# Optimization experiments

Hardware: AMD Instinct MI355X
Metric: run time of the kernel (lower is better)

Reference implementation:

```python
import jax, jax.numpy as jnp
import numpy as np


def setup_inputs() -> dict:
    key = jax.random.key(0)
    k1, k2, k3, k4 = jax.random.split(key, 4)
    N, E, IN, OUT = 100000, 1600000, 256, 32
    feat = jax.random.normal(k1, (N, IN), dtype=jnp.float32)
    src = jax.random.randint(k2, (E,), 0, N, dtype=jnp.int64)
    dst = jax.random.randint(k3, (E,), 0, N, dtype=jnp.int64)
    weight = jax.random.normal(k4, (IN, OUT), dtype=jnp.float32) * (6.0 / (IN + OUT)) ** 0.5
    bias = jnp.zeros((OUT,), dtype=jnp.float32)
    return {"feat": feat, "src": src, "dst": dst, "weight": weight, "bias": bias}


def reference(feat, src, dst, weight, bias):
    N = feat.shape[0]
    ones = jnp.ones(src.shape[0], dtype=feat.dtype)
    # norm='both': scale sources by out_degree^-0.5
    out_deg = jnp.clip(jax.ops.segment_sum(ones, src, num_segments=N), 1.0)
    feat = feat * (out_deg ** -0.5)[:, None]
    # in_feats (256) > out_feats (32): apply weight before aggregation
    feat = feat @ weight
    # SpMM: copy_src + sum over destination nodes
    rst = jax.ops.segment_sum(feat[src], dst, num_segments=N)  # [N, out]
    # scale destinations by in_degree^-0.5
    in_deg = jnp.clip(jax.ops.segment_sum(ones, dst, num_segments=N), 1.0)
    rst = rst * (in_deg ** -0.5)[:, None]
    rst = rst + bias
    return jax.nn.relu(rst)
```

## Files before the change

kernel.cpp:

```cpp
#include <hip/hip_runtime.h>
#include <hip/hip_bf16.h>


#define IN_F 256
#define OUT_F 32

#define G_ROWS 128
#define G_BK 32

#define BSHIFT 7
#define BNODES 128
#define NBK 1024
#define PB_EDGES 8192
#define AGG_CAP 4096


__global__ __launch_bounds__(1024) void hist_kernel(
    const int* __restrict__ src, const int* __restrict__ dst,
    unsigned short* __restrict__ mhistS, unsigned short* __restrict__ mhistD,
    int E) {
  __shared__ int hS[NBK], hD[NBK];
  int tid = threadIdx.x;
  hS[tid] = 0; hD[tid] = 0;
  __syncthreads();
  int e0 = blockIdx.x * PB_EDGES + tid * 8;
  if (e0 + 8 <= E) {
    int4 a0 = ((const int4*)(src + e0))[0], a1 = ((const int4*)(src + e0))[1];
    int4 b0 = ((const int4*)(dst + e0))[0], b1 = ((const int4*)(dst + e0))[1];
    int ss[8] = {a0.x, a0.y, a0.z, a0.w, a1.x, a1.y, a1.z, a1.w};
    int dd[8] = {b0.x, b0.y, b0.z, b0.w, b1.x, b1.y, b1.z, b1.w};
#pragma unroll
    for (int j = 0; j < 8; ++j) {
      atomicAdd(&hS[ss[j] >> BSHIFT], 1);
      atomicAdd(&hD[dd[j] >> BSHIFT], 1);
    }
  } else {
    for (int j = 0; j < 8; ++j) {
      int e = e0 + j;
      if (e < E) {
        atomicAdd(&hS[src[e] >> BSHIFT], 1);
        atomicAdd(&hD[dst[e] >> BSHIFT], 1);
      }
    }
  }
  __syncthreads();
  mhistS[blockIdx.x * NBK + tid] = (unsigned short)hS[tid];
  mhistD[blockIdx.x * NBK + tid] = (unsigned short)hD[tid];
}

__global__ __launch_bounds__(1024) void offset_kernel(
    unsigned short* __restrict__ mhistS, unsigned short* __restrict__ mhistD,
    int* __restrict__ baseS, int* __restrict__ baseD, int npb) {
  __shared__ int wsum[16];
  unsigned short* mh = blockIdx.x ? mhistD : mhistS;
  int* bb = blockIdx.x ? baseD : baseS;
  int b = threadIdx.x;
  int run = 0;
  int blk = 0;
  for (; blk + 4 <= npb; blk += 4) {
    int i0 = blk * NBK + b;
    int c0 = mh[i0];
    int c1 = mh[i0 + NBK];
    int c2 = mh[i0 + 2 * NBK];
    int c3 = mh[i0 + 3 * NBK];
    mh[i0] = (unsigned short)run;
    mh[i0 + NBK] = (unsigned short)(run + c0);
    mh[i0 + 2 * NBK] = (unsigned short)(run + c0 + c1);
    mh[i0 + 3 * NBK] = (unsigned short)(run + c0 + c1 + c2);
    run += c0 + c1 + c2 + c3;
  }
  for (; blk < npb; ++blk) {
    int idx = blk * NBK + b;
    int c = mh[idx];
    mh[idx] = (unsigned short)run;
    run += c;
  }
  int v = run, x = run;
#pragma unroll
  for (int d = 1; d < 64; d <<= 1) {
    int y = __shfl_up(x, d, 64);
    if ((b & 63) >= d) x += y;
  }
  if ((b & 63) == 63) wsum[b >> 6] = x;
  __syncthreads();
  int off = 0;
#pragma unroll
  for (int w = 0; w < 16; ++w)
    if (w < (b >> 6)) off += wsum[w];
  bb[b] = off + x - v;
  if (b == NBK - 1) bb[NBK] = off + x;
}

__global__ __launch_bounds__(1024) void partition_src_kernel(
    const int* __restrict__ src, const unsigned short* __restrict__ mbaseS,
    const int* __restrict__ baseS, unsigned char* __restrict__ pairs_s, int E) {
  __shared__ unsigned char sbuf[PB_EDGES];
  __shared__ int hist[NBK];
  __shared__ int lbase[NBK + 1];
  __shared__ int gbase[NBK];
  __shared__ int wsum[16];

  int tid = threadIdx.x;
  hist[tid] = 0;
  __syncthreads();

  int e0 = blockIdx.x * PB_EDGES + tid * 8;
  int myb[8], myslot[8];
  unsigned char mylow[8];
  if (e0 + 8 <= E) {
    int4 a0 = ((const int4*)(src + e0))[0], a1 = ((const int4*)(src + e0))[1];
    int ss[8] = {a0.x, a0.y, a0.z, a0.w, a1.x, a1.y, a1.z, a1.w};
#pragma unroll
    for (int j = 0; j < 8; ++j) {
      int b = ss[j] >> BSHIFT;
      myb[j] = b;
      mylow[j] = (unsigned char)(ss[j] & (BNODES - 1));
      myslot[j] = atomicAdd(&hist[b], 1);
    }
  } else {
#pragma unroll
    for (int j = 0; j < 8; ++j) {
      int e = e0 + j;
      if (e < E) {
        int s = src[e];
        int b = s >> BSHIFT;
        myb[j] = b;
        mylow[j] = (unsigned char)(s & (BNODES - 1));
        myslot[j] = atomicAdd(&hist[b], 1);
      } else {
        myb[j] = -1;
      }
    }
  }
  __syncthreads();

  {
    int v = hist[tid];
    int x = v;
#pragma unroll
    for (int d = 1; d < 64; d <<= 1) {
      int y = __shfl_up(x, d, 64);
      if ((tid & 63) >= d) x += y;
    }
    if ((tid & 63) == 63) wsum[tid >> 6] = x;
    __syncthreads();
    int off = 0;
#pragma unroll
    for (int w = 0; w < 16; ++w)
      if (w < (tid >> 6)) off += wsum[w];
    lbase[tid] = off + x - v;
    if (tid == NBK - 1) lbase[NBK] = off + x;
    gbase[tid] = baseS[tid] + (int)mbaseS[blockIdx.x * NBK + tid];
  }
  __syncthreads();

#pragma unroll
  for (int j = 0; j < 8; ++j)
    if (myb[j] >= 0) sbuf[lbase[myb[j]] + myslot[j]] = mylow[j];
  __syncthreads();

  int total = lbase[NBK];
  int idx = tid * 8;
  if (idx < total) {
    int lo = 0, hi = NBK;
    while (hi - lo > 1) {
      int mid = (lo + hi) >> 1;
      if (lbase[mid] <= idx) lo = mid; else hi = mid;
    }
    int b = lo;
#pragma unroll
    for (int j = 0; j < 8; ++j, ++idx) {
      if (idx >= total) break;
      while (idx >= lbase[b + 1]) ++b;
      pairs_s[gbase[b] + (idx - lbase[b])] = sbuf[idx];
    }
  }
}

__global__ __launch_bounds__(256) void src_count_kernel(
    const unsigned char* __restrict__ pairs_s, const int* __restrict__ baseS,
    float* __restrict__ scale_out, int N) {
  __shared__ int hist[BNODES];
  int tid = threadIdx.x;
  int b = blockIdx.x;
  if (tid < BNODES) hist[tid] = 0;
  __syncthreads();
  int s = baseS[b], e = baseS[b + 1];
  for (int i = s + tid; i < e; i += 256) atomicAdd(&hist[pairs_s[i]], 1);
  __syncthreads();
  if (tid < BNODES) {
    int node = (b << BSHIFT) + tid;
    if (node < N) {
      int c = hist[tid];
      scale_out[node] = (c < 1) ? 1.f : rsqrtf((float)c);
    }
  }
}

__device__ __forceinline__ void stage_tile(
    const float* __restrict__ feat, float* sf, int row0, int k0, int N,
    int tid) {
#pragma unroll
  for (int q = 0; q < 4; ++q) {
    int p = q * 256 + tid;
    int row = p >> 3;
    int c = (p & 7) ^ (row & 7);
    int g = row0 + row;
    if (g >= N) g = N - 1;
    const float* gp = feat + (size_t)g * IN_F + k0 + c * 4;
    __builtin_amdgcn_global_load_lds(
        (const __attribute__((address_space(1))) unsigned int*)gp,
        (__attribute__((address_space(3))) unsigned int*)(sf + p * 4),
        16, 0, 0);
  }
}

__global__ __launch_bounds__(256, 2) void gemm_kernel(
    const float* __restrict__ feat, const float* __restrict__ W,
    const float* __restrict__ scale_out, float* __restrict__ h, int N) {
  __shared__ float sW[IN_F * OUT_F];
  __shared__ float sF[2][G_ROWS * G_BK];
  __shared__ float sScale[G_ROWS];

  int tid = threadIdx.x;
  {
    const float4* W4 = (const float4*)W;
    float4* sW4 = (float4*)sW;
#pragma unroll
    for (int i = 0; i < 8; ++i) sW4[tid + i * 256] = W4[tid + i * 256];
  }
  int row0 = blockIdx.x * G_ROWS;
  if (tid < G_ROWS) {
    int gr = row0 + tid;
    sScale[tid] = (gr < N) ? scale_out[gr] : 0.f;
  }

  stage_tile(feat, &sF[0][0], row0, 0, N, tid);

  int tr = tid >> 3;
  int cg = (tid & 7) * 4;

  float acc[4][4];
#pragma unroll
  for (int i = 0; i < 4; ++i)
#pragma unroll
    for (int c = 0; c < 4; ++c) acc[i][c] = 0.f;

  __syncthreads();

  const int NT = IN_F / G_BK;
  for (int t = 0; t < NT; ++t) {
    if (t + 1 < NT)
      stage_tile(feat, &sF[(t + 1) & 1][0], row0, (t + 1) * G_BK, N, tid);

    const float* sf = &sF[t & 1][0];
    int kb = t * G_BK;
#pragma unroll
    for (int cc = 0; cc < 8; ++cc) {
      float4 a[4];
#pragma unroll
      for (int i = 0; i < 4; ++i) {
        int r = tr + 32 * i;
        int chunk = (r << 3) | (cc ^ (r & 7));
        a[i] = *(const float4*)(sf + chunk * 4);
      }
#pragma unroll
      for (int j = 0; j < 4; ++j) {
        float4 w = *(const float4*)(sW + (kb + cc * 4 + j) * OUT_F + cg);
#pragma unroll
        for (int i = 0; i < 4; ++i) {
          float aj = (j == 0) ? a[i].x : (j == 1) ? a[i].y
                   : (j == 2) ? a[i].z : a[i].w;
          acc[i][0] = fmaf(aj, w.x, acc[i][0]);
          acc[i][1] = fmaf(aj, w.y, acc[i][1]);
          acc[i][2] = fmaf(aj, w.z, acc[i][2]);
          acc[i][3] = fmaf(aj, w.w, acc[i][3]);
        }
      }
    }
    __syncthreads();
  }

#pragma unroll
  for (int i = 0; i < 4; ++i) {
    int r = tr + 32 * i;
    int g = row0 + r;
    if (g < N) {
      float s = sScale[r];
      float4 o = {acc[i][0] * s, acc[i][1] * s, acc[i][2] * s, acc[i][3] * s};
      *(float4*)(h + (size_t)g * OUT_F + cg) = o;
    }
  }
}

__global__ __launch_bounds__(1024) void partition_dst_kernel(
    const int* __restrict__ src, const int* __restrict__ dst,
    const unsigned short* __restrict__ mbaseD, const int* __restrict__ baseD,
    unsigned* __restrict__ pairs, int E) {
  __shared__ unsigned sbuf[PB_EDGES];
  __shared__ int hist[NBK];
  __shared__ int lbase[NBK + 1];
  __shared__ int gbase[NBK];
  __shared__ int wsum[16];

  int tid = threadIdx.x;
  hist[tid] = 0;
  __syncthreads();

  int e0 = blockIdx.x * PB_EDGES + tid * 8;
  int myb[8], myslot[8];
  unsigned mypk[8];
  if (e0 + 8 <= E) {
    int4 a0 = ((const int4*)(src + e0))[0], a1 = ((const int4*)(src + e0))[1];
    int4 b0 = ((const int4*)(dst + e0))[0], b1 = ((const int4*)(dst + e0))[1];
    int ss[8] = {a0.x, a0.y, a0.z, a0.w, a1.x, a1.y, a1.z, a1.w};
    int dd[8] = {b0.x, b0.y, b0.z, b0.w, b1.x, b1.y, b1.z, b1.w};
#pragma unroll
    for (int j = 0; j < 8; ++j) {
      int b = dd[j] >> BSHIFT;
      myb[j] = b;
      mypk[j] = (unsigned)ss[j] | ((unsigned)(dd[j] & (BNODES - 1)) << 17);
      myslot[j] = atomicAdd(&hist[b], 1);
    }
  } else {
#pragma unroll
    for (int j = 0; j < 8; ++j) {
      int e = e0 + j;
      if (e < E) {
        int s = src[e], d = dst[e];
        int b = d >> BSHIFT;
        myb[j] = b;
        mypk[j] = (unsigned)s | ((unsigned)(d & (BNODES - 1)) << 17);
        myslot[j] = atomicAdd(&hist[b], 1);
      } else {
        myb[j] = -1;
      }
    }
  }
  __syncthreads();

  {
    int v = hist[tid];
    int x = v;
#pragma unroll
    for (int d = 1; d < 64; d <<= 1) {
      int y = __shfl_up(x, d, 64);
      if ((tid & 63) >= d) x += y;
    }
    if ((tid & 63) == 63) wsum[tid >> 6] = x;
    __syncthreads();
    int off = 0;
#pragma unroll
    for (int w = 0; w < 16; ++w)
      if (w < (tid >> 6)) off += wsum[w];
    lbase[tid] = off + x - v;
    if (tid == NBK - 1) lbase[NBK] = off + x;
    gbase[tid] = baseD[tid] + (int)mbaseD[blockIdx.x * NBK + tid];
  }
  __syncthreads();

#pragma unroll
  for (int j = 0; j < 8; ++j)
    if (myb[j] >= 0) sbuf[lbase[myb[j]] + myslot[j]] = mypk[j];
  __syncthreads();

  int total = lbase[NBK];
  int idx = tid * 8;
  if (idx < total) {
    int lo = 0, hi = NBK;
    while (hi - lo > 1) {
      int mid = (lo + hi) >> 1;
      if (lbase[mid] <= idx) lo = mid; else hi = mid;
    }
    int b = lo;
#pragma unroll
    for (int j = 0; j < 8; ++j, ++idx) {
      if (idx >= total) break;
      while (idx >= lbase[b + 1]) ++b;
      pairs[gbase[b] + (idx - lbase[b])] = sbuf[idx];
    }
  }
}

__global__ __launch_bounds__(256) void sort_agg_kernel(
    const unsigned* __restrict__ pairs, const int* __restrict__ baseD,
    const float* __restrict__ h, const float* __restrict__ bias,
    float* __restrict__ out, int N) {
  __shared__ unsigned spk[AGG_CAP];
  __shared__ int hist[BNODES];
  __shared__ int rs[BNODES + 1];
  __shared__ int wsum2[4];

  int tid = threadIdx.x;
  int lane = tid & 31;
  int eg = tid >> 5;
  int b = blockIdx.x;
  int start = baseD[b];
  int end = baseD[b + 1];

  float acc[16];
  int degc[16];
#pragma unroll
  for (int t = 0; t < 16; ++t) { acc[t] = 0.f; degc[t] = 0; }

  for (int chunk = start; chunk < end; chunk += AGG_CAP) {
    int cnt = min(end - chunk, AGG_CAP);
    if (tid < BNODES) hist[tid] = 0;
    __syncthreads();

    unsigned mypk[16];
    int myslot[16];
    int nmine = 0;
    for (int i = tid; i < cnt; i += 256) {
      unsigned pk = pairs[chunk + i];
      mypk[nmine] = pk;
      myslot[nmine] = atomicAdd(&hist[pk >> 17], 1);
      ++nmine;
    }
    __syncthreads();

    {
      int v = (tid < BNODES) ? hist[tid] : 0;
      int x = v;
#pragma unroll
      for (int d = 1; d < 64; d <<= 1) {
        int y = __shfl_up(x, d, 64);
        if ((tid & 63) >= d) x += y;
      }
      if ((tid & 63) == 63) wsum2[tid >> 6] = x;
      __syncthreads();
      int off = (tid >= 64 && tid < BNODES) ? wsum2[0] : 0;
      if (tid < BNODES) rs[tid] = off + x - v;
      if (tid == BNODES - 1) rs[BNODES] = off + x;
    }
    __syncthreads();

    for (int i = 0; i < nmine; ++i) {
      unsigned pk = mypk[i];
      spk[rs[pk >> 17] + myslot[i]] = pk;
    }
    __syncthreads();

#pragma unroll 1
    for (int t = 0; t < 16; ++t) {
      int n = eg * 16 + t;
      int a = rs[n], bnd = rs[n + 1];
      degc[t] += bnd - a;
      float s = acc[t];
      int j = a;
      for (; j + 8 <= bnd; j += 8) {
        unsigned p0 = spk[j], p1 = spk[j + 1], p2 = spk[j + 2], p3 = spk[j + 3];
        unsigned p4 = spk[j + 4], p5 = spk[j + 5], p6 = spk[j + 6], p7 = spk[j + 7];
        float f0 = h[(size_t)(p0 & 0x1FFFF) * OUT_F + lane];
        float f1 = h[(size_t)(p1 & 0x1FFFF) * OUT_F + lane];
        float f2 = h[(size_t)(p2 & 0x1FFFF) * OUT_F + lane];
        float f3 = h[(size_t)(p3 & 0x1FFFF) * OUT_F + lane];
        float f4 = h[(size_t)(p4 & 0x1FFFF) * OUT_F + lane];
        float f5 = h[(size_t)(p5 & 0x1FFFF) * OUT_F + lane];
        float f6 = h[(size_t)(p6 & 0x1FFFF) * OUT_F + lane];
        float f7 = h[(size_t)(p7 & 0x1FFFF) * OUT_F + lane];
        s += ((f0 + f1) + (f2 + f3)) + ((f4 + f5) + (f6 + f7));
      }
      if (j + 4 <= bnd) {
        unsigned p0 = spk[j], p1 = spk[j + 1], p2 = spk[j + 2], p3 = spk[j + 3];
        float f0 = h[(size_t)(p0 & 0x1FFFF) * OUT_F + lane];
        float f1 = h[(size_t)(p1 & 0x1FFFF) * OUT_F + lane];
        float f2 = h[(size_t)(p2 & 0x1FFFF) * OUT_F + lane];
        float f3 = h[(size_t)(p3 & 0x1FFFF) * OUT_F + lane];
        s += (f0 + f1) + (f2 + f3);
        j += 4;
      }
      for (; j < bnd; ++j)
        s += h[(size_t)(spk[j] & 0x1FFFF) * OUT_F + lane];
      acc[t] = s;
    }
    __syncthreads();
  }

  int node0 = b << BSHIFT;
#pragma unroll
  for (int t = 0; t < 16; ++t) {
    int node = node0 + eg * 16 + t;
    if (node < N) {
      float sc = degc[t] > 0 ? rsqrtf((float)degc[t]) : 1.f;
      out[(size_t)node * OUT_F + lane] = fmaxf(fmaf(acc[t], sc, bias[lane]), 0.f);
    }
  }
}

__global__ __launch_bounds__(256) void degree_kernel(
    const int* __restrict__ src, const int* __restrict__ dst,
    int* __restrict__ cnt_out, int* __restrict__ cnt_in, int E) {
  int i = blockIdx.x * 256 + threadIdx.x;
  if (i < E) {
    atomicAdd(cnt_out + src[i], 1);
    atomicAdd(cnt_in + dst[i], 1);
  }
}

__global__ __launch_bounds__(256) void cnt_to_scale_kernel(
    const int* __restrict__ cnt, float* __restrict__ scale, int N) {
  int i = blockIdx.x * 256 + threadIdx.x;
  if (i < N) {
    int c = cnt[i];
    scale[i] = (c < 1) ? 1.f : rsqrtf((float)c);
  }
}

__global__ __launch_bounds__(256) void aggregate_kernel(
    const int* __restrict__ src, const int* __restrict__ dst,
    const float* __restrict__ h, float* __restrict__ out, int E) {
  int lane = threadIdx.x & 31;
  int e = (blockIdx.x * 256 + threadIdx.x) >> 5;
  if (e >= E) return;
  float v = h[(size_t)src[e] * OUT_F + lane];
  unsafeAtomicAdd(out + (size_t)dst[e] * OUT_F + lane, v);
}

__global__ __launch_bounds__(256) void finalize_kernel(
    float* __restrict__ out, const int* __restrict__ cnt_in,
    const float* __restrict__ bias, int N) {
  int idx = blockIdx.x * 256 + threadIdx.x;
  if (idx >= N * 8) return;
  int n = idx >> 3;
  int o = (idx & 7) * 4;
  float dg = (float)cnt_in[n];
  float s = dg < 1.f ? 1.f : rsqrtf(dg);
  float4 bv = *(const float4*)(bias + o);
  float4 v = ((const float4*)out)[idx];
  v.x = fmaxf(fmaf(v.x, s, bv.x), 0.f);
  v.y = fmaxf(fmaf(v.y, s, bv.y), 0.f);
  v.z = fmaxf(fmaf(v.z, s, bv.z), 0.f);
  v.w = fmaxf(fmaf(v.w, s, bv.w), 0.f);
  ((float4*)out)[idx] = v;
}

extern "C" void kernel_launch(void* const* d_in, const int* in_sizes, int n_in,
                              void* d_out, int out_size, void* d_ws, size_t ws_size,
                              hipStream_t stream) {
  const float* feat = (const float*)d_in[0];
  const int* src = (const int*)d_in[1];
  const int* dst = (const int*)d_in[2];
  const float* weight = (const float*)d_in[3];
  const float* bias = (const float*)d_in[4];
  float* out = (float*)d_out;

  int N = in_sizes[0] / IN_F;
  int E = in_sizes[1];
  int nb = (N + BNODES - 1) >> BSHIFT;
  int npb = (E + PB_EDGES - 1) / PB_EDGES;

  float* h = (float*)d_ws;
  unsigned* pairs = (unsigned*)(h + (size_t)N * OUT_F);
  unsigned char* pairs_s = (unsigned char*)pairs;
  unsigned short* mhistS = (unsigned short*)(pairs + E);
  unsigned short* mhistD = mhistS + (size_t)npb * NBK;
  int* baseS = (int*)(mhistD + (size_t)npb * NBK);
  int* baseD = baseS + NBK + 1;
  float* scale_out = (float*)(baseD + NBK + 1);

  size_t need = ((size_t)N * OUT_F + (size_t)E + (size_t)N + 2 * (NBK + 1)) * 4 +
                (size_t)npb * NBK * 2 * 2;
  bool fast = (ws_size >= need) && (N <= (1 << 17)) && (nb <= NBK);

  if (fast) {
    hist_kernel<<<npb, 1024, 0, stream>>>(src, dst, mhistS, mhistD, E);
    offset_kernel<<<2, 1024, 0, stream>>>(mhistS, mhistD, baseS, baseD, npb);
    partition_src_kernel<<<npb, 1024, 0, stream>>>(src, mhistS, baseS, pairs_s, E);
    src_count_kernel<<<nb, 256, 0, stream>>>(pairs_s, baseS, scale_out, N);
    gemm_kernel<<<(N + G_ROWS - 1) / G_ROWS, 256, 0, stream>>>(
        feat, weight, scale_out, h, N);
    partition_dst_kernel<<<npb, 1024, 0, stream>>>(src, dst, mhistD, baseD, pairs, E);
    sort_agg_kernel<<<nb, 256, 0, stream>>>(pairs, baseD, h, bias, out, N);
  } else {
    int* cnt_out = (int*)(h + (size_t)N * OUT_F);
    int* cnt_in = cnt_out + N;
    float* scl = (float*)(cnt_in + N);
    hipMemsetAsync(cnt_out, 0, (size_t)2 * N * sizeof(int), stream);
    hipMemsetAsync(out, 0, (size_t)N * OUT_F * sizeof(float), stream);
    degree_kernel<<<(E + 255) / 256, 256, 0, stream>>>(src, dst, cnt_out, cnt_in, E);
    cnt_to_scale_kernel<<<(N + 255) / 256, 256, 0, stream>>>(cnt_out, scl, N);
    gemm_kernel<<<(N + G_ROWS - 1) / G_ROWS, 256, 0, stream>>>(feat, weight, scl, h, N);
    aggregate_kernel<<<(E + 7) / 8, 256, 0, stream>>>(src, dst, h, out, E);
    finalize_kernel<<<(N * 8 + 255) / 256, 256, 0, stream>>>(out, cnt_in, bias, N);
  }
}
```

Measured before the change: 288.5 us.

## Give each wave private double-buffered feature tiles and drop block barriers in GEMM

The GEMM now splits each 128-row block into four 32-row wave slices. Each wave stages its own 16-wide K tiles into private double-buffered LDS with global_load_lds and waits with explicit s_waitcnt vmcnt instead of a block-wide __syncthreads each step. The K tile is halved and the occupancy hint is raised from 2 to 4 blocks, aiming at more overlap between loads and FMA work. The cost is twice as many loop iterations with smaller tiles, and correctness now depends on per-wave waitcnt ordering rather than barriers. LDS per block (about 49 KB) may also cap real occupancy below the hint.

```diff
diff --git a/kernel.cpp b/kernel.cpp
--- a/kernel.cpp
+++ b/kernel.cpp
@@ -6,7 +6,9 @@
 #define OUT_F 32
 
 #define G_ROWS 128
-#define G_BK 32
+#define G_BK 16
+#define W_ROWS 32
+#define G_NT (IN_F / G_BK)
 
 #define BSHIFT 7
 #define BNODES 128
@@ -197,48 +199,50 @@
   }
 }
 
-__device__ __forceinline__ void stage_tile(
-    const float* __restrict__ feat, float* sf, int row0, int k0, int N,
-    int tid) {
-#pragma unroll
-  for (int q = 0; q < 4; ++q) {
-    int p = q * 256 + tid;
-    int row = p >> 3;
-    int c = (p & 7) ^ (row & 7);
-    int g = row0 + row;
-    if (g >= N) g = N - 1;
-    const float* gp = feat + (size_t)g * IN_F + k0 + c * 4;
-    __builtin_amdgcn_global_load_lds(
-        (const __attribute__((address_space(1))) unsigned int*)gp,
-        (__attribute__((address_space(3))) unsigned int*)(sf + p * 4),
-        16, 0, 0);
-  }
-}
-
-__global__ __launch_bounds__(256, 2) void gemm_kernel(
+__global__ __launch_bounds__(256, 4) void gemm_kernel(
     const float* __restrict__ feat, const float* __restrict__ W,
     const float* __restrict__ scale_out, float* __restrict__ h, int N) {
   __shared__ float sW[IN_F * OUT_F];
-  __shared__ float sF[2][G_ROWS * G_BK];
+  __shared__ float sF[4][2][W_ROWS * G_BK];
   __shared__ float sScale[G_ROWS];
 
   int tid = threadIdx.x;
+  int wv = tid >> 6;
+  int lane = tid & 63;
   {
     const float4* W4 = (const float4*)W;
     float4* sW4 = (float4*)sW;
 #pragma unroll
     for (int i = 0; i < 8; ++i) sW4[tid + i * 256] = W4[tid + i * 256];
   }
-  int row0 = blockIdx.x * G_ROWS;
+  int grow = blockIdx.x * G_ROWS;
   if (tid < G_ROWS) {
-    int gr = row0 + tid;
+    int gr = grow + tid;
     sScale[tid] = (gr < N) ? scale_out[gr] : 0.f;
   }
-
-  stage_tile(feat, &sF[0][0], row0, 0, N, tid);
-
-  int tr = tid >> 3;
-  int cg = (tid & 7) * 4;
+  int wrow0 = grow + wv * W_ROWS;
+
+  auto stage = [&](int t) {
+    int k0 = t * G_BK;
+    float* dstb = &sF[wv][t & 1][0];
+#pragma unroll
+    for (int q = 0; q < 2; ++q) {
+      int r = q * 16 + (lane >> 2);
+      int c = (lane & 3) ^ (r & 3);
+      int g = wrow0 + r;
+      if (g >= N) g = N - 1;
+      const float* gp = feat + (size_t)g * IN_F + k0 + c * 4;
+      __builtin_amdgcn_global_load_lds(
+          (const __attribute__((address_space(1))) unsigned int*)gp,
+          (__attribute__((address_space(3))) unsigned int*)(dstb + q * 256 + lane * 4),
+          16, 0, 0);
+    }
+  };
+
+  stage(0);
+
+  int tr = lane >> 3;
+  int cg = (lane & 7) * 4;
 
   float acc[4][4];
 #pragma unroll
@@ -248,21 +252,23 @@
 
   __syncthreads();
 
-  const int NT = IN_F / G_BK;
-  for (int t = 0; t < NT; ++t) {
-    if (t + 1 < NT)
-      stage_tile(feat, &sF[(t + 1) & 1][0], row0, (t + 1) * G_BK, N, tid);
-
-    const float* sf = &sF[t & 1][0];
+  for (int t = 0; t < G_NT; ++t) {
+    if (t + 1 < G_NT) {
+      stage(t + 1);
+      asm volatile("s_waitcnt vmcnt(2)" ::: "memory");
+    } else {
+      asm volatile("s_waitcnt vmcnt(0)" ::: "memory");
+    }
+
+    const float* sf = &sF[wv][t & 1][0];
     int kb = t * G_BK;
 #pragma unroll
-    for (int cc = 0; cc < 8; ++cc) {
+    for (int cc = 0; cc < 4; ++cc) {
       float4 a[4];
 #pragma unroll
       for (int i = 0; i < 4; ++i) {
-        int r = tr + 32 * i;
-        int chunk = (r << 3) | (cc ^ (r & 7));
-        a[i] = *(const float4*)(sf + chunk * 4);
+        int r = tr + 8 * i;
+        a[i] = *(const float4*)(sf + r * 16 + ((cc ^ (r & 3)) << 2));
       }
 #pragma unroll
       for (int j = 0; j < 4; ++j) {
@@ -278,15 +284,14 @@
         }
       }
     }
-    __syncthreads();
   }
 
 #pragma unroll
   for (int i = 0; i < 4; ++i) {
-    int r = tr + 32 * i;
-    int g = row0 + r;
+    int r = tr + 8 * i;
+    int g = wrow0 + r;
     if (g < N) {
-      float s = sScale[r];
+      float s = sScale[wv * W_ROWS + r];
       float4 o = {acc[i][0] * s, acc[i][1] * s, acc[i][2] * s, acc[i][3] * s};
       *(float4*)(h + (size_t)g * OUT_F + cg) = o;
     }
```

New measurement: 279.6 us. -3.1%, faster.
